# Kernel tuning notes

Hardware: AMD Instinct MI355X
Metric: run time of the kernel (lower is better)

Reference implementation:

```python
import jax, jax.numpy as jnp
import numpy as np
from itertools import permutations

SIZES = (16, 32, 32, 32)  # token_sizes for layout dims (v, t, h, w)
N = SIZES[0] * SIZES[1] * SIZES[2] * SIZES[3]  # num_tokens = 524288
B = 32
EPS = 1e-3


def setup_inputs() -> dict:
    key = jax.random.key(0)
    ks = jax.random.split(key, 12)
    u = lambda k, shape: jax.random.uniform(k, shape, dtype=jnp.float32)
    alphas = [1.0, 2.0, 4.0]
    comps = np.array(
        [[alphas[v], alphas[t], alphas[hw], alphas[hw]]
         for v, t, hw in permutations(range(3), 3)], dtype=np.float32)  # [6, 4]
    return {
        "components": jnp.asarray(comps),
        "u_rate_src": u(ks[0], (1,)),
        "u_rate_tgt": u(ks[1], (1,)),
        "u0_src": u(ks[2], (B, N)),
        "u0_tgt": u(ks[3], (B, N)),
        "u_v_src": u(ks[4], (B, SIZES[0])),
        "u_t_src": u(ks[5], (B, SIZES[1])),
        "u_h_src": u(ks[6], (B, SIZES[2])),
        "u_w_src": u(ks[7], (B, SIZES[3])),
        "u_v_tgt": u(ks[8], (B, SIZES[0])),
        "u_t_tgt": u(ks[9], (B, SIZES[1])),
        "u_h_tgt": u(ks[10], (B, SIZES[2])),
        "u_w_tgt": u(ks[11], (B, SIZES[3])),
        "idx": 2,
    }


def _clamp(x):
    return jnp.clip(x, EPS, 1.0 - EPS)


def _binary_mask(u_rate, u0, u_dims, alphas):
    # event_prior: log-prob per token = log U0 + sum_dim log(U_dim)/alpha_dim (broadcast over pattern)
    P = jnp.log(_clamp(u0))  # [B, N]
    for i, ud in enumerate(u_dims):
        shape = [B, 1, 1, 1, 1]
        shape[1 + i] = SIZES[i]
        rep = jnp.broadcast_to(
            (jnp.log(_clamp(ud)) / alphas[i]).reshape(shape),
            (B,) + SIZES).reshape(B, N)
        P = P + rep
    # rate_prior: one shared uniform, K = floor(U * N), expanded over batch
    K = (_clamp(u_rate) * N).astype(jnp.int32)  # [1]
    K = jnp.broadcast_to(K, (B,))[:, None]  # [B, 1]
    # binary_topk_: rank via double argsort (0 = largest), mask = K > rank
    rank = jnp.argsort(jnp.argsort(-P, axis=-1), axis=-1)
    return K > rank


def reference(components, u_rate_src, u_rate_tgt, u0_src, u0_tgt,
              u_v_src, u_t_src, u_h_src, u_w_src,
              u_v_tgt, u_t_tgt, u_h_tgt, u_w_tgt, idx):
    alphas = components[idx]  # [4], one alpha per layout dim, shared by src/tgt
    src = _binary_mask(u_rate_src, u0_src,
                       (u_v_src, u_t_src, u_h_src, u_w_src), alphas)
    tgt = _binary_mask(u_rate_tgt, u0_tgt,
                       (u_v_tgt, u_t_tgt, u_h_tgt, u_w_tgt), alphas)
    return src, tgt
```

## Files before the change

### kernel.cpp

```cpp
#include <hip/hip_runtime.h>
#include <stdint.h>

#define NTOK 524288
#define ROWS 64
#define CHUNKS 64
#define NTHR 256
#define F4_PER_ROW (NTOK / 4)
#define F4_PER_CHUNK (F4_PER_ROW / CHUNKS)
#define F4_PER_THR (F4_PER_CHUNK / NTHR)
#define GCAP 8192

#define OFF_H1   0u
#define OFF_H2   (OFF_H1 + ROWS * 4096u * 4u)
#define OFF_B1   (OFF_H2 + ROWS * 4096u * 4u)
#define OFF_CG   (OFF_B1 + ROWS * 4u)
#define OFF_B2   (OFF_CG + ROWS * 4u)
#define OFF_REM  (OFF_B2 + ROWS * 4u)
#define OFF_IT   (OFF_REM + ROWS * 4u)
#define OFF_GCNT (OFF_IT + ROWS * 4u)
#define OFF_T    (OFF_GCNT + ROWS * 4u)
#define OFF_ZERO_END (OFF_T + ROWS * 8u)
#define OFF_TAB  OFF_ZERO_END
#define OFF_GKEY (OFF_TAB + ROWS * 112u * 8u)
#define OFF_GIDX (OFF_GKEY + ROWS * (unsigned)GCAP * 8u)
#define WS_NEED  (OFF_GIDX + ROWS * (unsigned)GCAP * 4u)

__device__ __forceinline__ double clamp64(double x) {
  return fmin(fmax(x, 1.0e-3), 1.0 - 1.0e-3);
}

__device__ __forceinline__ unsigned compute_K(float ur) {
  float urf = fminf(fmaxf(ur, 1.0e-3f), 1.0f - 1.0e-3f);
  return (unsigned)(int)(urf * (float)NTOK);
}

__global__ void k_tables(const float* __restrict__ comps, const int* __restrict__ idxp,
                         const float* __restrict__ uvs, const float* __restrict__ uts,
                         const float* __restrict__ uhs, const float* __restrict__ uws,
                         const float* __restrict__ uvt, const float* __restrict__ utt,
                         const float* __restrict__ uht, const float* __restrict__ uwt,
                         double* __restrict__ tabs) {
  int idx = idxp[0];
  double alpha[4];
  for (int d = 0; d < 4; ++d) alpha[d] = (double)comps[idx * 4 + d];
  for (int i = threadIdx.x; i < ROWS * 112; i += blockDim.x) {
    int row = i / 112, j = i % 112;
    int m = row >> 5, b = row & 31;
    int d, jj, dsz;
    if (j < 16)      { d = 0; jj = j;      dsz = 16; }
    else if (j < 48) { d = 1; jj = j - 16; dsz = 32; }
    else if (j < 80) { d = 2; jj = j - 48; dsz = 32; }
    else             { d = 3; jj = j - 80; dsz = 32; }
    const float* u;
    if (m == 0) u = (d == 0) ? uvs : (d == 1) ? uts : (d == 2) ? uhs : uws;
    else        u = (d == 0) ? uvt : (d == 1) ? utt : (d == 2) ? uht : uwt;
    double x = clamp64((double)u[b * dsz + jj]);
    double a = alpha[d];
    double f;
    if (a == 1.0)      f = x;
    else if (a == 2.0) f = sqrt(x);
    else if (a == 4.0) f = sqrt(sqrt(x));
    else               f = pow(x, 1.0 / a);
    tabs[row * 112 + j] = f;
  }
}

__global__ void k_hist1(const float* __restrict__ u0s, const float* __restrict__ u0t,
                        const double* __restrict__ tabs, unsigned int* __restrict__ gh1) {
  __shared__ double tb[112];
  __shared__ unsigned int h[4096];
  int row = blockIdx.x / CHUNKS, chunk = blockIdx.x % CHUNKS;
  for (int i = threadIdx.x; i < 112; i += blockDim.x) tb[i] = tabs[row * 112 + i];
  for (int i = threadIdx.x; i < 4096; i += blockDim.x) h[i] = 0;
  __syncthreads();
  int m = row >> 5, b = row & 31;
  const float4* u0 = reinterpret_cast<const float4*>((m ? u0t : u0s) + (size_t)b * NTOK);
  int base = chunk * F4_PER_CHUNK;
  for (int it = 0; it < F4_PER_THR; ++it) {
    int f4 = base + it * NTHR + threadIdx.x;
    float4 x = u0[f4];
    int n0 = f4 * 4;
    int w0 = n0 & 31, hh = (n0 >> 5) & 31, tt = (n0 >> 10) & 31, vv = n0 >> 15;
    double g = tb[vv] * tb[16 + tt] * tb[48 + hh];
    double k0 = clamp64((double)x.x) * (g * tb[80 + w0 + 0]);
    double k1 = clamp64((double)x.y) * (g * tb[80 + w0 + 1]);
    double k2 = clamp64((double)x.z) * (g * tb[80 + w0 + 2]);
    double k3 = clamp64((double)x.w) * (g * tb[80 + w0 + 3]);
    atomicAdd(&h[(unsigned)((unsigned long long)__double_as_longlong(k0) >> 51) & 0xFFFu], 1u);
    atomicAdd(&h[(unsigned)((unsigned long long)__double_as_longlong(k1) >> 51) & 0xFFFu], 1u);
    atomicAdd(&h[(unsigned)((unsigned long long)__double_as_longlong(k2) >> 51) & 0xFFFu], 1u);
    atomicAdd(&h[(unsigned)((unsigned long long)__double_as_longlong(k3) >> 51) & 0xFFFu], 1u);
  }
  __syncthreads();
  for (int i = threadIdx.x; i < 4096; i += blockDim.x) {
    unsigned c = h[i];
    if (c) atomicAdd(&gh1[row * 4096 + i], c);
  }
}

__global__ __launch_bounds__(256) void k_scan1(const unsigned int* __restrict__ gh1,
                                               const float* __restrict__ urs,
                                               const float* __restrict__ urt,
                                               int* __restrict__ sB1, int* __restrict__ sCG) {
  __shared__ unsigned suf[256];
  __shared__ int best;
  int row = blockIdx.x;
  int t = threadIdx.x;
  const unsigned* h = gh1 + row * 4096;
  unsigned loc[16]; unsigned own = 0;
#pragma unroll
  for (int i = 0; i < 16; ++i) { loc[i] = h[t * 16 + i]; own += loc[i]; }
  suf[t] = own;
  if (t == 0) best = -1;
  __syncthreads();
  for (int off = 1; off < 256; off <<= 1) {
    unsigned add = (t + off < 256) ? suf[t + off] : 0u;
    __syncthreads();
    suf[t] += add;
    __syncthreads();
  }
  int m = row >> 5;
  unsigned K = compute_K(m ? urt[0] : urs[0]);
  unsigned above = suf[t] - own;
  int cand = -1;
  unsigned cum = above;
  for (int i = 15; i >= 0; --i) {
    if (cum + loc[i] >= K) { cand = t * 16 + i; break; }
    cum += loc[i];
  }
  if (cand >= 0) atomicMax(&best, cand);
  __syncthreads();
  int bb = best;
  if (bb >= 0 && (bb >> 4) == t) {
    unsigned cg = above;
    for (int i = 15; i > (bb & 15); --i) cg += loc[i];
    sB1[row] = bb;
    sCG[row] = (int)cg;
  }
}

__global__ void k_hist2(const float* __restrict__ u0s, const float* __restrict__ u0t,
                        const double* __restrict__ tabs, const int* __restrict__ sB1,
                        unsigned int* __restrict__ gh2) {
  __shared__ double tb[112];
  __shared__ unsigned int h[4096];
  int row = blockIdx.x / CHUNKS, chunk = blockIdx.x % CHUNKS;
  for (int i = threadIdx.x; i < 112; i += blockDim.x) tb[i] = tabs[row * 112 + i];
  for (int i = threadIdx.x; i < 4096; i += blockDim.x) h[i] = 0;
  __syncthreads();
  unsigned b1 = (unsigned)sB1[row];
  int m = row >> 5, b = row & 31;
  const float4* u0 = reinterpret_cast<const float4*>((m ? u0t : u0s) + (size_t)b * NTOK);
  int base = chunk * F4_PER_CHUNK;
  for (int it = 0; it < F4_PER_THR; ++it) {
    int f4 = base + it * NTHR + threadIdx.x;
    float4 x = u0[f4];
    int n0 = f4 * 4;
    int w0 = n0 & 31, hh = (n0 >> 5) & 31, tt = (n0 >> 10) & 31, vv = n0 >> 15;
    double g = tb[vv] * tb[16 + tt] * tb[48 + hh];
    double ks[4];
    ks[0] = clamp64((double)x.x) * (g * tb[80 + w0 + 0]);
    ks[1] = clamp64((double)x.y) * (g * tb[80 + w0 + 1]);
    ks[2] = clamp64((double)x.z) * (g * tb[80 + w0 + 2]);
    ks[3] = clamp64((double)x.w) * (g * tb[80 + w0 + 3]);
#pragma unroll
    for (int c = 0; c < 4; ++c) {
      unsigned long long kb = (unsigned long long)__double_as_longlong(ks[c]);
      if (((unsigned)(kb >> 51) & 0xFFFu) == b1)
        atomicAdd(&h[(unsigned)(kb >> 39) & 0xFFFu], 1u);
    }
  }
  __syncthreads();
  for (int i = threadIdx.x; i < 4096; i += blockDim.x) {
    unsigned c = h[i];
    if (c) atomicAdd(&gh2[row * 4096 + i], c);
  }
}

__global__ __launch_bounds__(256) void k_scan2(const unsigned int* __restrict__ gh2,
                                               const float* __restrict__ urs,
                                               const float* __restrict__ urt,
                                               const int* __restrict__ sCG,
                                               int* __restrict__ sB2, int* __restrict__ sREM) {
  __shared__ unsigned suf[256];
  __shared__ int best;
  int row = blockIdx.x;
  int t = threadIdx.x;
  const unsigned* h = gh2 + row * 4096;
  unsigned loc[16]; unsigned own = 0;
#pragma unroll
  for (int i = 0; i < 16; ++i) { loc[i] = h[t * 16 + i]; own += loc[i]; }
  suf[t] = own;
  if (t == 0) best = -1;
  __syncthreads();
  for (int off = 1; off < 256; off <<= 1) {
    unsigned add = (t + off < 256) ? suf[t + off] : 0u;
    __syncthreads();
    suf[t] += add;
    __syncthreads();
  }
  int m = row >> 5;
  unsigned K = compute_K(m ? urt[0] : urs[0]);
  unsigned K2 = K - (unsigned)sCG[row];
  unsigned above = suf[t] - own;
  int cand = -1;
  unsigned cum = above;
  for (int i = 15; i >= 0; --i) {
    if (cum + loc[i] >= K2) { cand = t * 16 + i; break; }
    cum += loc[i];
  }
  if (cand >= 0) atomicMax(&best, cand);
  __syncthreads();
  int bb = best;
  if (bb >= 0 && (bb >> 4) == t) {
    unsigned a2 = above;
    for (int i = 15; i > (bb & 15); --i) a2 += loc[i];
    sB2[row] = bb;
    sREM[row] = (int)(K2 - a2);
  }
}

__global__ void k_gather(const float* __restrict__ u0s, const float* __restrict__ u0t,
                         const double* __restrict__ tabs,
                         const int* __restrict__ sB1, const int* __restrict__ sB2,
                         unsigned int* __restrict__ gcnt,
                         unsigned long long* __restrict__ gkey, unsigned int* __restrict__ gidx) {
  __shared__ double tb[112];
  int row = blockIdx.x / CHUNKS, chunk = blockIdx.x % CHUNKS;
  for (int i = threadIdx.x; i < 112; i += blockDim.x) tb[i] = tabs[row * 112 + i];
  __syncthreads();
  unsigned pref = ((unsigned)sB1[row] << 12) | (unsigned)sB2[row];
  int m = row >> 5, b = row & 31;
  const float4* u0 = reinterpret_cast<const float4*>((m ? u0t : u0s) + (size_t)b * NTOK);
  int base = chunk * F4_PER_CHUNK;
  for (int it = 0; it < F4_PER_THR; ++it) {
    int f4 = base + it * NTHR + threadIdx.x;
    float4 x = u0[f4];
    int n0 = f4 * 4;
    int w0 = n0 & 31, hh = (n0 >> 5) & 31, tt = (n0 >> 10) & 31, vv = n0 >> 15;
    double g = tb[vv] * tb[16 + tt] * tb[48 + hh];
    double ks[4];
    ks[0] = clamp64((double)x.x) * (g * tb[80 + w0 + 0]);
    ks[1] = clamp64((double)x.y) * (g * tb[80 + w0 + 1]);
    ks[2] = clamp64((double)x.z) * (g * tb[80 + w0 + 2]);
    ks[3] = clamp64((double)x.w) * (g * tb[80 + w0 + 3]);
#pragma unroll
    for (int c = 0; c < 4; ++c) {
      unsigned long long kb = (unsigned long long)__double_as_longlong(ks[c]);
      if (((unsigned)(kb >> 39) & 0xFFFFFFu) == pref) {
        unsigned pos = atomicAdd(&gcnt[row], 1u);
        if (pos < GCAP) {
          gkey[(size_t)row * GCAP + pos] = kb;
          gidx[(size_t)row * GCAP + pos] = (unsigned)(n0 + c);
        }
      }
    }
  }
}

__global__ __launch_bounds__(1024) void k_select(const unsigned long long* __restrict__ gkey,
                                                 const unsigned int* __restrict__ gidx,
                                                 const unsigned int* __restrict__ gcnt,
                                                 const int* __restrict__ sREM,
                                                 unsigned long long* __restrict__ sT,
                                                 int* __restrict__ sIT) {
  __shared__ unsigned long long k[GCAP];
  __shared__ unsigned int ix[GCAP];
  int row = blockIdx.x;
  unsigned n_r = gcnt[row];
  if (n_r > GCAP) n_r = GCAP;
  unsigned n2 = 2;
  while (n2 < n_r) n2 <<= 1;
  for (int i = threadIdx.x; i < (int)n2; i += blockDim.x) {
    if ((unsigned)i < n_r) { k[i] = gkey[(size_t)row * GCAP + i]; ix[i] = gidx[(size_t)row * GCAP + i]; }
    else                   { k[i] = 0ULL; ix[i] = 0xFFFFFFFFu; }
  }
  __syncthreads();
  for (unsigned kk = 2; kk <= n2; kk <<= 1) {
    for (unsigned j = kk >> 1; j > 0; j >>= 1) {
      for (int i = threadIdx.x; i < (int)n2; i += blockDim.x) {
        int pj = i ^ (int)j;
        if (pj > i) {
          unsigned long long k1 = k[i], k2 = k[pj];
          unsigned i1 = ix[i], i2 = ix[pj];
          bool bef = (k1 > k2) || (k1 == k2 && i1 < i2);
          bool dirAsc = ((i & (int)kk) == 0);
          if (bef != dirAsc) { k[i] = k2; k[pj] = k1; ix[i] = i2; ix[pj] = i1; }
        }
      }
      __syncthreads();
    }
  }
  if (threadIdx.x == 0) {
    int rem = sREM[row];
    if (rem < 1) rem = 1;
    if ((unsigned)rem > n_r) rem = (int)n_r;
    sT[row] = k[rem - 1];
    sIT[row] = (int)ix[rem - 1];
  }
}

__global__ void k_final(const float* __restrict__ u0s, const float* __restrict__ u0t,
                        const double* __restrict__ tabs,
                        const unsigned long long* __restrict__ sT, const int* __restrict__ sIT,
                        int* __restrict__ out) {
  __shared__ double tb[112];
  int row = blockIdx.x / CHUNKS, chunk = blockIdx.x % CHUNKS;
  for (int i = threadIdx.x; i < 112; i += blockDim.x) tb[i] = tabs[row * 112 + i];
  __syncthreads();
  unsigned long long T = sT[row];
  int IT = sIT[row];
  int m = row >> 5, b = row & 31;
  const float4* u0 = reinterpret_cast<const float4*>((m ? u0t : u0s) + (size_t)b * NTOK);
  int4* o = reinterpret_cast<int4*>(out + (size_t)row * NTOK);
  int base = chunk * F4_PER_CHUNK;
  for (int it = 0; it < F4_PER_THR; ++it) {
    int f4 = base + it * NTHR + threadIdx.x;
    float4 x = u0[f4];
    int n0 = f4 * 4;
    int w0 = n0 & 31, hh = (n0 >> 5) & 31, tt = (n0 >> 10) & 31, vv = n0 >> 15;
    double g = tb[vv] * tb[16 + tt] * tb[48 + hh];
    unsigned long long kb0 = (unsigned long long)__double_as_longlong(clamp64((double)x.x) * (g * tb[80 + w0 + 0]));
    unsigned long long kb1 = (unsigned long long)__double_as_longlong(clamp64((double)x.y) * (g * tb[80 + w0 + 1]));
    unsigned long long kb2 = (unsigned long long)__double_as_longlong(clamp64((double)x.z) * (g * tb[80 + w0 + 2]));
    unsigned long long kb3 = (unsigned long long)__double_as_longlong(clamp64((double)x.w) * (g * tb[80 + w0 + 3]));
    int4 r;
    r.x = (kb0 > T || (kb0 == T && (n0 + 0) <= IT)) ? 1 : 0;
    r.y = (kb1 > T || (kb1 == T && (n0 + 1) <= IT)) ? 1 : 0;
    r.z = (kb2 > T || (kb2 == T && (n0 + 2) <= IT)) ? 1 : 0;
    r.w = (kb3 > T || (kb3 == T && (n0 + 3) <= IT)) ? 1 : 0;
    o[f4] = r;
  }
}

extern "C" void kernel_launch(void* const* d_in, const int* in_sizes, int n_in,
                              void* d_out, int out_size, void* d_ws, size_t ws_size,
                              hipStream_t stream) {
  const float* comps = (const float*)d_in[0];
  const float* urs   = (const float*)d_in[1];
  const float* urt   = (const float*)d_in[2];
  const float* u0s   = (const float*)d_in[3];
  const float* u0t   = (const float*)d_in[4];
  const float* uvs   = (const float*)d_in[5];
  const float* uts   = (const float*)d_in[6];
  const float* uhs   = (const float*)d_in[7];
  const float* uws   = (const float*)d_in[8];
  const float* uvt   = (const float*)d_in[9];
  const float* utt   = (const float*)d_in[10];
  const float* uht   = (const float*)d_in[11];
  const float* uwt   = (const float*)d_in[12];
  const int*   idxp  = (const int*)d_in[13];
  int* out = (int*)d_out;

  char* ws = (char*)d_ws;
  unsigned int*       gh1  = (unsigned int*)(ws + OFF_H1);
  unsigned int*       gh2  = (unsigned int*)(ws + OFF_H2);
  int*                sB1  = (int*)(ws + OFF_B1);
  int*                sCG  = (int*)(ws + OFF_CG);
  int*                sB2  = (int*)(ws + OFF_B2);
  int*                sREM = (int*)(ws + OFF_REM);
  int*                sIT  = (int*)(ws + OFF_IT);
  unsigned int*       gcnt = (unsigned int*)(ws + OFF_GCNT);
  unsigned long long* sT   = (unsigned long long*)(ws + OFF_T);
  double*             tabs = (double*)(ws + OFF_TAB);
  unsigned long long* gkey = (unsigned long long*)(ws + OFF_GKEY);
  unsigned int*       gidx = (unsigned int*)(ws + OFF_GIDX);

  hipMemsetAsync(d_ws, 0, OFF_ZERO_END, stream);

  k_tables<<<1, 256, 0, stream>>>(comps, idxp, uvs, uts, uhs, uws, uvt, utt, uht, uwt, tabs);
  k_hist1<<<ROWS * CHUNKS, NTHR, 0, stream>>>(u0s, u0t, tabs, gh1);
  k_scan1<<<ROWS, 256, 0, stream>>>(gh1, urs, urt, sB1, sCG);
  k_hist2<<<ROWS * CHUNKS, NTHR, 0, stream>>>(u0s, u0t, tabs, sB1, gh2);
  k_scan2<<<ROWS, 256, 0, stream>>>(gh2, urs, urt, sCG, sB2, sREM);
  k_gather<<<ROWS * CHUNKS, NTHR, 0, stream>>>(u0s, u0t, tabs, sB1, sB2, gcnt, gkey, gidx);
  k_select<<<ROWS, 1024, 0, stream>>>(gkey, gidx, gcnt, sREM, sT, sIT);
  k_final<<<ROWS * CHUNKS, NTHR, 0, stream>>>(u0s, u0t, tabs, sT, sIT, out);
}
```

Baseline: 377.9 us.

## Capture first-bucket candidates during hist2 to skip the full gather pass

The second histogram pass now also stages every element in the selected first-level bucket (key and index) into shared memory and flushes it to a per-row global buffer. The select kernel then filters that buffer by the second-level bucket, so the third full read of the 128 MB input is skipped; the old full-scan gather remains only as a fallback when a row's bucket overflows its capacity. Separately, the first histogram uses two interleaved shared-memory copies to reduce atomic contention. The cost is extra atomics and writes in hist2, a larger workspace, and fallback blocks that still launch and exit early.

```diff
diff --git a/kernel.cpp b/kernel.cpp
--- a/kernel.cpp
+++ b/kernel.cpp
@@ -9,21 +9,26 @@
 #define F4_PER_CHUNK (F4_PER_ROW / CHUNKS)
 #define F4_PER_THR (F4_PER_CHUNK / NTHR)
 #define GCAP 8192
+#define CB1CAP 131072
+#define STAGECAP 2048
+#define FB_CHUNKS 16
 
 #define OFF_H1   0u
 #define OFF_H2   (OFF_H1 + ROWS * 4096u * 4u)
 #define OFF_B1   (OFF_H2 + ROWS * 4096u * 4u)
-#define OFF_CG   (OFF_B1 + ROWS * 4u)
-#define OFF_B2   (OFF_CG + ROWS * 4u)
-#define OFF_REM  (OFF_B2 + ROWS * 4u)
-#define OFF_IT   (OFF_REM + ROWS * 4u)
-#define OFF_GCNT (OFF_IT + ROWS * 4u)
-#define OFF_T    (OFF_GCNT + ROWS * 4u)
-#define OFF_ZERO_END (OFF_T + ROWS * 8u)
+#define OFF_CG   (OFF_B1 + 256u)
+#define OFF_B2   (OFF_CG + 256u)
+#define OFF_REM  (OFF_B2 + 256u)
+#define OFF_IT   (OFF_REM + 256u)
+#define OFF_GCNT (OFF_IT + 256u)
+#define OFF_BCNT (OFF_GCNT + 256u)
+#define OFF_T    (OFF_BCNT + 256u)
+#define OFF_ZERO_END (OFF_T + 512u)
 #define OFF_TAB  OFF_ZERO_END
-#define OFF_GKEY (OFF_TAB + ROWS * 112u * 8u)
-#define OFF_GIDX (OFF_GKEY + ROWS * (unsigned)GCAP * 8u)
-#define WS_NEED  (OFF_GIDX + ROWS * (unsigned)GCAP * 4u)
+#define OFF_BK   (OFF_TAB + ROWS * 112u * 8u)
+#define OFF_BI   (OFF_BK + (size_t)ROWS * CB1CAP * 8u)
+#define OFF_GKEY (OFF_BI + (size_t)ROWS * CB1CAP * 4u)
+#define OFF_GIDX (OFF_GKEY + (size_t)ROWS * GCAP * 8u)
 
 __device__ __forceinline__ double clamp64(double x) {
   return fmin(fmax(x, 1.0e-3), 1.0 - 1.0e-3);
@@ -68,11 +73,12 @@
 __global__ void k_hist1(const float* __restrict__ u0s, const float* __restrict__ u0t,
                         const double* __restrict__ tabs, unsigned int* __restrict__ gh1) {
   __shared__ double tb[112];
-  __shared__ unsigned int h[4096];
+  __shared__ unsigned int h[2 * 4100];
   int row = blockIdx.x / CHUNKS, chunk = blockIdx.x % CHUNKS;
   for (int i = threadIdx.x; i < 112; i += blockDim.x) tb[i] = tabs[row * 112 + i];
-  for (int i = threadIdx.x; i < 4096; i += blockDim.x) h[i] = 0;
-  __syncthreads();
+  for (int i = threadIdx.x; i < 2 * 4100; i += blockDim.x) h[i] = 0;
+  __syncthreads();
+  unsigned rep = (threadIdx.x & 1) * 4100u;
   int m = row >> 5, b = row & 31;
   const float4* u0 = reinterpret_cast<const float4*>((m ? u0t : u0s) + (size_t)b * NTOK);
   int base = chunk * F4_PER_CHUNK;
@@ -86,14 +92,14 @@
     double k1 = clamp64((double)x.y) * (g * tb[80 + w0 + 1]);
     double k2 = clamp64((double)x.z) * (g * tb[80 + w0 + 2]);
     double k3 = clamp64((double)x.w) * (g * tb[80 + w0 + 3]);
-    atomicAdd(&h[(unsigned)((unsigned long long)__double_as_longlong(k0) >> 51) & 0xFFFu], 1u);
-    atomicAdd(&h[(unsigned)((unsigned long long)__double_as_longlong(k1) >> 51) & 0xFFFu], 1u);
-    atomicAdd(&h[(unsigned)((unsigned long long)__double_as_longlong(k2) >> 51) & 0xFFFu], 1u);
-    atomicAdd(&h[(unsigned)((unsigned long long)__double_as_longlong(k3) >> 51) & 0xFFFu], 1u);
+    atomicAdd(&h[rep + ((unsigned)((unsigned long long)__double_as_longlong(k0) >> 51) & 0xFFFu)], 1u);
+    atomicAdd(&h[rep + ((unsigned)((unsigned long long)__double_as_longlong(k1) >> 51) & 0xFFFu)], 1u);
+    atomicAdd(&h[rep + ((unsigned)((unsigned long long)__double_as_longlong(k2) >> 51) & 0xFFFu)], 1u);
+    atomicAdd(&h[rep + ((unsigned)((unsigned long long)__double_as_longlong(k3) >> 51) & 0xFFFu)], 1u);
   }
   __syncthreads();
   for (int i = threadIdx.x; i < 4096; i += blockDim.x) {
-    unsigned c = h[i];
+    unsigned c = h[i] + h[4100 + i];
     if (c) atomicAdd(&gh1[row * 4096 + i], c);
   }
 }
@@ -139,14 +145,21 @@
   }
 }
 
-__global__ void k_hist2(const float* __restrict__ u0s, const float* __restrict__ u0t,
-                        const double* __restrict__ tabs, const int* __restrict__ sB1,
-                        unsigned int* __restrict__ gh2) {
+__global__ void k_hist2g(const float* __restrict__ u0s, const float* __restrict__ u0t,
+                         const double* __restrict__ tabs, const int* __restrict__ sB1,
+                         unsigned int* __restrict__ gh2,
+                         unsigned int* __restrict__ bcnt,
+                         unsigned long long* __restrict__ bk, unsigned int* __restrict__ bi) {
   __shared__ double tb[112];
   __shared__ unsigned int h[4096];
+  __shared__ unsigned long long sk[STAGECAP];
+  __shared__ unsigned int si[STAGECAP];
+  __shared__ unsigned int scnt;
+  __shared__ unsigned int sbase;
   int row = blockIdx.x / CHUNKS, chunk = blockIdx.x % CHUNKS;
   for (int i = threadIdx.x; i < 112; i += blockDim.x) tb[i] = tabs[row * 112 + i];
   for (int i = threadIdx.x; i < 4096; i += blockDim.x) h[i] = 0;
+  if (threadIdx.x == 0) scnt = 0;
   __syncthreads();
   unsigned b1 = (unsigned)sB1[row];
   int m = row >> 5, b = row & 31;
@@ -166,11 +179,32 @@
 #pragma unroll
     for (int c = 0; c < 4; ++c) {
       unsigned long long kb = (unsigned long long)__double_as_longlong(ks[c]);
-      if (((unsigned)(kb >> 51) & 0xFFFu) == b1)
+      if (((unsigned)(kb >> 51) & 0xFFFu) == b1) {
         atomicAdd(&h[(unsigned)(kb >> 39) & 0xFFFu], 1u);
-    }
-  }
-  __syncthreads();
+        unsigned p = atomicAdd(&scnt, 1u);
+        if (p < STAGECAP) { sk[p] = kb; si[p] = (unsigned)(n0 + c); }
+        else {
+          unsigned gp = atomicAdd(&bcnt[row], 1u);
+          if (gp < CB1CAP) {
+            bk[(size_t)row * CB1CAP + gp] = kb;
+            bi[(size_t)row * CB1CAP + gp] = (unsigned)(n0 + c);
+          }
+        }
+      }
+    }
+  }
+  __syncthreads();
+  unsigned nst = scnt; if (nst > STAGECAP) nst = STAGECAP;
+  if (threadIdx.x == 0) sbase = atomicAdd(&bcnt[row], nst);
+  __syncthreads();
+  unsigned bs = sbase;
+  for (unsigned i = threadIdx.x; i < nst; i += blockDim.x) {
+    unsigned gp = bs + i;
+    if (gp < CB1CAP) {
+      bk[(size_t)row * CB1CAP + gp] = sk[i];
+      bi[(size_t)row * CB1CAP + gp] = si[i];
+    }
+  }
   for (int i = threadIdx.x; i < 4096; i += blockDim.x) {
     unsigned c = h[i];
     if (c) atomicAdd(&gh2[row * 4096 + i], c);
@@ -220,20 +254,22 @@
   }
 }
 
-__global__ void k_gather(const float* __restrict__ u0s, const float* __restrict__ u0t,
-                         const double* __restrict__ tabs,
-                         const int* __restrict__ sB1, const int* __restrict__ sB2,
-                         unsigned int* __restrict__ gcnt,
-                         unsigned long long* __restrict__ gkey, unsigned int* __restrict__ gidx) {
+__global__ void k_gather_fb(const float* __restrict__ u0s, const float* __restrict__ u0t,
+                            const double* __restrict__ tabs,
+                            const int* __restrict__ sB1, const int* __restrict__ sB2,
+                            const unsigned int* __restrict__ bcnt,
+                            unsigned int* __restrict__ gcnt,
+                            unsigned long long* __restrict__ gkey, unsigned int* __restrict__ gidx) {
+  int row = blockIdx.x / FB_CHUNKS, chunk = blockIdx.x % FB_CHUNKS;
+  if (bcnt[row] <= CB1CAP) return;
   __shared__ double tb[112];
-  int row = blockIdx.x / CHUNKS, chunk = blockIdx.x % CHUNKS;
   for (int i = threadIdx.x; i < 112; i += blockDim.x) tb[i] = tabs[row * 112 + i];
   __syncthreads();
   unsigned pref = ((unsigned)sB1[row] << 12) | (unsigned)sB2[row];
   int m = row >> 5, b = row & 31;
   const float4* u0 = reinterpret_cast<const float4*>((m ? u0t : u0s) + (size_t)b * NTOK);
-  int base = chunk * F4_PER_CHUNK;
-  for (int it = 0; it < F4_PER_THR; ++it) {
+  int base = chunk * (F4_PER_ROW / FB_CHUNKS);
+  for (int it = 0; it < F4_PER_ROW / FB_CHUNKS / NTHR; ++it) {
     int f4 = base + it * NTHR + threadIdx.x;
     float4 x = u0[f4];
     int n0 = f4 * 4;
@@ -258,22 +294,48 @@
   }
 }
 
-__global__ __launch_bounds__(1024) void k_select(const unsigned long long* __restrict__ gkey,
+__global__ __launch_bounds__(1024) void k_select(const unsigned long long* __restrict__ bk,
+                                                 const unsigned int* __restrict__ bi,
+                                                 const unsigned int* __restrict__ bcnt,
+                                                 const unsigned long long* __restrict__ gkey,
                                                  const unsigned int* __restrict__ gidx,
                                                  const unsigned int* __restrict__ gcnt,
+                                                 const int* __restrict__ sB2,
                                                  const int* __restrict__ sREM,
                                                  unsigned long long* __restrict__ sT,
                                                  int* __restrict__ sIT) {
   __shared__ unsigned long long k[GCAP];
   __shared__ unsigned int ix[GCAP];
+  __shared__ unsigned int lcnt;
   int row = blockIdx.x;
-  unsigned n_r = gcnt[row];
-  if (n_r > GCAP) n_r = GCAP;
+  if (threadIdx.x == 0) lcnt = 0;
+  __syncthreads();
+  unsigned cnt1 = bcnt[row];
+  unsigned n_r;
+  if (cnt1 <= CB1CAP) {
+    unsigned b2 = (unsigned)sB2[row];
+    for (unsigned i = threadIdx.x; i < cnt1; i += blockDim.x) {
+      unsigned long long kb = bk[(size_t)row * CB1CAP + i];
+      if (((unsigned)(kb >> 39) & 0xFFFu) == b2) {
+        unsigned p = atomicAdd(&lcnt, 1u);
+        if (p < GCAP) { k[p] = kb; ix[p] = bi[(size_t)row * CB1CAP + i]; }
+      }
+    }
+    __syncthreads();
+    n_r = lcnt; if (n_r > GCAP) n_r = GCAP;
+  } else {
+    n_r = gcnt[row];
+    if (n_r > GCAP) n_r = GCAP;
+    for (unsigned i = threadIdx.x; i < n_r; i += blockDim.x) {
+      k[i] = gkey[(size_t)row * GCAP + i];
+      ix[i] = gidx[(size_t)row * GCAP + i];
+    }
+    __syncthreads();
+  }
   unsigned n2 = 2;
   while (n2 < n_r) n2 <<= 1;
-  for (int i = threadIdx.x; i < (int)n2; i += blockDim.x) {
-    if ((unsigned)i < n_r) { k[i] = gkey[(size_t)row * GCAP + i]; ix[i] = gidx[(size_t)row * GCAP + i]; }
-    else                   { k[i] = 0ULL; ix[i] = 0xFFFFFFFFu; }
+  for (unsigned i = threadIdx.x; i < n2; i += blockDim.x) {
+    if (i >= n_r) { k[i] = 0ULL; ix[i] = 0xFFFFFFFFu; }
   }
   __syncthreads();
   for (unsigned kk = 2; kk <= n2; kk <<= 1) {
@@ -361,8 +423,11 @@
   int*                sREM = (int*)(ws + OFF_REM);
   int*                sIT  = (int*)(ws + OFF_IT);
   unsigned int*       gcnt = (unsigned int*)(ws + OFF_GCNT);
+  unsigned int*       bcnt = (unsigned int*)(ws + OFF_BCNT);
   unsigned long long* sT   = (unsigned long long*)(ws + OFF_T);
   double*             tabs = (double*)(ws + OFF_TAB);
+  unsigned long long* bk   = (unsigned long long*)(ws + OFF_BK);
+  unsigned int*       bi   = (unsigned int*)(ws + OFF_BI);
   unsigned long long* gkey = (unsigned long long*)(ws + OFF_GKEY);
   unsigned int*       gidx = (unsigned int*)(ws + OFF_GIDX);
 
@@ -371,9 +436,9 @@
   k_tables<<<1, 256, 0, stream>>>(comps, idxp, uvs, uts, uhs, uws, uvt, utt, uht, uwt, tabs);
   k_hist1<<<ROWS * CHUNKS, NTHR, 0, stream>>>(u0s, u0t, tabs, gh1);
   k_scan1<<<ROWS, 256, 0, stream>>>(gh1, urs, urt, sB1, sCG);
-  k_hist2<<<ROWS * CHUNKS, NTHR, 0, stream>>>(u0s, u0t, tabs, sB1, gh2);
+  k_hist2g<<<ROWS * CHUNKS, NTHR, 0, stream>>>(u0s, u0t, tabs, sB1, gh2, bcnt, bk, bi);
   k_scan2<<<ROWS, 256, 0, stream>>>(gh2, urs, urt, sCG, sB2, sREM);
-  k_gather<<<ROWS * CHUNKS, NTHR, 0, stream>>>(u0s, u0t, tabs, sB1, sB2, gcnt, gkey, gidx);
-  k_select<<<ROWS, 1024, 0, stream>>>(gkey, gidx, gcnt, sREM, sT, sIT);
+  k_gather_fb<<<ROWS * FB_CHUNKS, NTHR, 0, stream>>>(u0s, u0t, tabs, sB1, sB2, bcnt, gcnt, gkey, gidx);
+  k_select<<<ROWS, 1024, 0, stream>>>(bk, bi, bcnt, gkey, gidx, gcnt, sB2, sREM, sT, sIT);
   k_final<<<ROWS * CHUNKS, NTHR, 0, stream>>>(u0s, u0t, tabs, sT, sIT, out);
 }
```

Measured after the change: 401.4 us. 6.2% more time.
